# Kernel tuning notes

Measured on AMD Instinct MI355X. Metric: run time of the kernel, lower is better.

## Reference

```python
import jax, jax.numpy as jnp
import numpy as np

E, T, H, I = 16, 512, 1024, 4096


def setup_inputs() -> dict:
    key = jax.random.key(0)
    k_x, k_w1, k_b1, k_w2, k_b2 = jax.random.split(key, 5)
    scale = 0.02
    return {
        "route_results": jax.random.normal(k_x, (E, T, H), dtype=jnp.float32),
        "W1": jax.random.normal(k_w1, (E, H, I), dtype=jnp.float32) * scale,
        "b1": jax.random.normal(k_b1, (E, I), dtype=jnp.float32) * scale,
        "W2": jax.random.normal(k_w2, (E, I, H), dtype=jnp.float32) * scale,
        "b2": jax.random.normal(k_b2, (E, H), dtype=jnp.float32) * scale,
    }


def reference(route_results, W1, b1, W2, b2):
    # Per-expert 2-layer linear MLP (no activation in source), expressed as
    # a single grouped (batched) GEMM over the expert axis e.
    h = jnp.einsum("eth,ehi->eti", route_results, W1) + b1[:, None, :]
    y = jnp.einsum("eti,eih->eth", h, W2) + b2[:, None, :]
    # torch.cat(expert_results, dim=0): stack expert outputs along token dim.
    e, t, hid = y.shape
    return y.reshape(e * t, hid)
```

## Files before the change

kernel.cpp:

```cpp
#include <hip/hip_runtime.h>
#include <stdint.h>


#define E_ 16
#define T_ 512
#define H_ 1024
#define I_ 4096

typedef _Float16 f16x8 __attribute__((ext_vector_type(8)));
typedef __fp16   h2    __attribute__((ext_vector_type(2)));
typedef float    f32x4 __attribute__((ext_vector_type(4)));

#define LDK 40

__device__ __forceinline__ void lds_barrier() {
    __builtin_amdgcn_sched_barrier(0);
    asm volatile("s_waitcnt lgkmcnt(0)" ::: "memory");
    __builtin_amdgcn_sched_barrier(0);
    __builtin_amdgcn_s_barrier();
    __builtin_amdgcn_sched_barrier(0);
}

template <bool A_IS_F16, bool OUT_IS_F16>
__global__ __launch_bounds__(256, 2) void moe_gemm(const void* __restrict__ Aall,
                                                   const float* __restrict__ Ball,
                                                   const float* __restrict__ biasAll,
                                                   void* __restrict__ Call,
                                                   int M, int N, int K) {
    __shared__ _Float16 sA[2][128 * LDK];
    __shared__ _Float16 sB[2][128 * LDK];

    const int e   = blockIdx.z;
    const int m0  = blockIdx.y * 128;
    const int n0  = blockIdx.x * 128;
    const int tid = threadIdx.x;
    const int lane = tid & 63;
    const int wave = tid >> 6;
    const int wm = (wave >> 1) * 64;
    const int wn = (wave & 1) * 64;
    const int lrow = lane & 15;
    const int lk8  = (lane >> 4) * 8;

    const float* B_e    = Ball + (size_t)e * K * N;
    const float* bias_e = biasAll + (size_t)e * N;
    const float*     A_f32 = (const float*)Aall + (size_t)e * M * K;
    const _Float16*  A_f16 = (const _Float16*)Aall + (size_t)e * M * K;

    const int bn  = ((tid >> 6) & 1) * 64 + (tid & 63);
    const int bkh = (tid >> 7) * 16;
    const int ar = (tid >> 6) * 32 + ((tid & 63) >> 2);
    const int ak = (tid & 3) * 8;
    const int r  = tid >> 2;
    const int c8 = (tid & 3) * 8;

    float bv[16];
    f32x4 a32[4];
    f16x8 a16[2];

    auto load_tile = [&](int k0) {
        const float* bsrc = B_e + (size_t)(k0 + bkh) * N + n0 + bn;
#pragma unroll
        for (int kk = 0; kk < 16; ++kk)
            bv[kk] = bsrc[(size_t)kk * N];
        if (A_IS_F16) {
            a16[0] = *(const f16x8*)(A_f16 + (size_t)(m0 + r) * K + k0 + c8);
            a16[1] = *(const f16x8*)(A_f16 + (size_t)(m0 + r + 64) * K + k0 + c8);
        } else {
            const float* a0 = A_f32 + (size_t)(m0 + ar) * K + k0 + ak;
            a32[0] = *(const f32x4*)a0;
            a32[1] = *(const f32x4*)(a0 + 4);
            const float* a1 = A_f32 + (size_t)(m0 + ar + 16) * K + k0 + ak;
            a32[2] = *(const f32x4*)a1;
            a32[3] = *(const f32x4*)(a1 + 4);
        }
    };

    auto store_tile = [&](_Float16* dA, _Float16* dB) {
        f16x8 w0, w1;
#pragma unroll
        for (int j = 0; j < 4; ++j) {
            ((h2*)&w0)[j] = __builtin_amdgcn_cvt_pkrtz(bv[2 * j],     bv[2 * j + 1]);
            ((h2*)&w1)[j] = __builtin_amdgcn_cvt_pkrtz(bv[8 + 2 * j], bv[8 + 2 * j + 1]);
        }
        *(f16x8*)&dB[bn * LDK + bkh]     = w0;
        *(f16x8*)&dB[bn * LDK + bkh + 8] = w1;
        if (A_IS_F16) {
            *(f16x8*)&dA[r * LDK + c8]        = a16[0];
            *(f16x8*)&dA[(r + 64) * LDK + c8] = a16[1];
        } else {
#pragma unroll
            for (int p = 0; p < 2; ++p) {
                f16x8 w;
                ((h2*)&w)[0] = __builtin_amdgcn_cvt_pkrtz(a32[2 * p].x, a32[2 * p].y);
                ((h2*)&w)[1] = __builtin_amdgcn_cvt_pkrtz(a32[2 * p].z, a32[2 * p].w);
                ((h2*)&w)[2] = __builtin_amdgcn_cvt_pkrtz(a32[2 * p + 1].x, a32[2 * p + 1].y);
                ((h2*)&w)[3] = __builtin_amdgcn_cvt_pkrtz(a32[2 * p + 1].z, a32[2 * p + 1].w);
                *(f16x8*)&dA[(ar + p * 16) * LDK + ak] = w;
            }
        }
    };

    f32x4 acc[4][4];
    const f32x4 zero = {0.f, 0.f, 0.f, 0.f};
#pragma unroll
    for (int i = 0; i < 4; ++i)
#pragma unroll
        for (int j = 0; j < 4; ++j) acc[i][j] = zero;

    const int nt = K / 32;

    load_tile(0);
    store_tile(sA[0], sB[0]);
    load_tile(32);
    lds_barrier();

    for (int t = 0; t < nt; ++t) {
        const int cur = t & 1;
        const _Float16* rA = sA[cur];
        const _Float16* rB = sB[cur];

        f16x8 af[4], bf[4];
#pragma unroll
        for (int mi = 0; mi < 4; ++mi)
            af[mi] = *(const f16x8*)&rA[(wm + mi * 16 + lrow) * LDK + lk8];
#pragma unroll
        for (int ni = 0; ni < 4; ++ni)
            bf[ni] = *(const f16x8*)&rB[(wn + ni * 16 + lrow) * LDK + lk8];

#pragma unroll
        for (int mi = 0; mi < 2; ++mi)
#pragma unroll
            for (int ni = 0; ni < 4; ++ni)
                acc[mi][ni] = __builtin_amdgcn_mfma_f32_16x16x32_f16(af[mi], bf[ni], acc[mi][ni], 0, 0, 0);

        if (t + 1 < nt) {
            store_tile(sA[cur ^ 1], sB[cur ^ 1]);
            if (t + 2 < nt)
                load_tile((t + 2) * 32);
        }

#pragma unroll
        for (int mi = 2; mi < 4; ++mi)
#pragma unroll
            for (int ni = 0; ni < 4; ++ni)
                acc[mi][ni] = __builtin_amdgcn_mfma_f32_16x16x32_f16(af[mi], bf[ni], acc[mi][ni], 0, 0, 0);

        lds_barrier();
    }

    const int row_base = (lane >> 4) * 4;
#pragma unroll
    for (int ni = 0; ni < 4; ++ni) {
        const int n = n0 + wn + ni * 16 + lrow;
        const float bv2 = bias_e[n];
#pragma unroll
        for (int mi = 0; mi < 4; ++mi) {
            const int mbase = m0 + wm + mi * 16 + row_base;
#pragma unroll
            for (int rr = 0; rr < 4; ++rr) {
                const float val = acc[mi][ni][rr] + bv2;
                const size_t idx = (size_t)e * M * N + (size_t)(mbase + rr) * N + n;
                if (OUT_IS_F16)
                    ((_Float16*)Call)[idx] = (_Float16)val;
                else
                    ((float*)Call)[idx] = val;
            }
        }
    }
}

extern "C" void kernel_launch(void* const* d_in, const int* in_sizes, int n_in,
                              void* d_out, int out_size, void* d_ws, size_t ws_size,
                              hipStream_t stream) {
    (void)in_sizes; (void)n_in; (void)out_size; (void)ws_size;
    const float* x  = (const float*)d_in[0];
    const float* W1 = (const float*)d_in[1];
    const float* b1 = (const float*)d_in[2];
    const float* W2 = (const float*)d_in[3];
    const float* b2 = (const float*)d_in[4];
    float* out = (float*)d_out;
    _Float16* hbuf = (_Float16*)d_ws;

    dim3 blk(256, 1, 1);
    dim3 g1(I_ / 128, T_ / 128, E_);
    moe_gemm<false, true><<<g1, blk, 0, stream>>>((const void*)x, W1, b1, (void*)hbuf, T_, I_, H_);
    dim3 g2(H_ / 128, T_ / 128, E_);
    moe_gemm<true, false><<<g2, blk, 0, stream>>>((const void*)hbuf, W2, b2, (void*)out, T_, H_, I_);
}
```

Measured before the change: 695.8 us.

## Single-buffer LDS, raise occupancy, and use 64-row tiles for second GEMM

Replaces the double-buffered LDS pipeline with a single buffer and two barriers per k-step, so the LDS store of the next tile no longer overlaps the MFMA work. Launch bounds go from 2 to 4 blocks per CU, and the second GEMM uses BM=64 tiles, doubling its grid from 512 to 1024 blocks. The aim is better occupancy and wave parallelism on the second GEMM, at the cost of an extra barrier per iteration, lost intra-block overlap, and lower B-tile reuse per block.

```diff
diff --git a/kernel.cpp b/kernel.cpp
--- a/kernel.cpp
+++ b/kernel.cpp
@@ -21,22 +21,25 @@
     __builtin_amdgcn_sched_barrier(0);
 }
 
-template <bool A_IS_F16, bool OUT_IS_F16>
-__global__ __launch_bounds__(256, 2) void moe_gemm(const void* __restrict__ Aall,
+template <int BM, bool A_IS_F16, bool OUT_IS_F16>
+__global__ __launch_bounds__(256, 4) void moe_gemm(const void* __restrict__ Aall,
                                                    const float* __restrict__ Ball,
                                                    const float* __restrict__ biasAll,
                                                    void* __restrict__ Call,
                                                    int M, int N, int K) {
-    __shared__ _Float16 sA[2][128 * LDK];
-    __shared__ _Float16 sB[2][128 * LDK];
+    constexpr int MFRAG = BM / 32;
+    constexpr int AP    = BM / 64;
+
+    __shared__ _Float16 sA[BM * LDK];
+    __shared__ _Float16 sB[128 * LDK];
 
     const int e   = blockIdx.z;
-    const int m0  = blockIdx.y * 128;
+    const int m0  = blockIdx.y * BM;
     const int n0  = blockIdx.x * 128;
     const int tid = threadIdx.x;
     const int lane = tid & 63;
     const int wave = tid >> 6;
-    const int wm = (wave >> 1) * 64;
+    const int wm = (wave >> 1) * (BM / 2);
     const int wn = (wave & 1) * 64;
     const int lrow = lane & 15;
     const int lk8  = (lane >> 4) * 8;
@@ -46,16 +49,16 @@
     const float*     A_f32 = (const float*)Aall + (size_t)e * M * K;
     const _Float16*  A_f16 = (const _Float16*)Aall + (size_t)e * M * K;
 
-    const int bn  = ((tid >> 6) & 1) * 64 + (tid & 63);
+    const int bn  = tid & 127;
     const int bkh = (tid >> 7) * 16;
+    const int r  = tid >> 2;
+    const int c8 = (tid & 3) * 8;
     const int ar = (tid >> 6) * 32 + ((tid & 63) >> 2);
     const int ak = (tid & 3) * 8;
-    const int r  = tid >> 2;
-    const int c8 = (tid & 3) * 8;
 
     float bv[16];
-    f32x4 a32[4];
-    f16x8 a16[2];
+    f32x4 a32[2 * AP];
+    f16x8 a16[AP];
 
     auto load_tile = [&](int k0) {
         const float* bsrc = B_e + (size_t)(k0 + bkh) * N + n0 + bn;
@@ -63,102 +66,96 @@
         for (int kk = 0; kk < 16; ++kk)
             bv[kk] = bsrc[(size_t)kk * N];
         if (A_IS_F16) {
-            a16[0] = *(const f16x8*)(A_f16 + (size_t)(m0 + r) * K + k0 + c8);
-            a16[1] = *(const f16x8*)(A_f16 + (size_t)(m0 + r + 64) * K + k0 + c8);
+#pragma unroll
+            for (int p = 0; p < AP; ++p)
+                a16[p] = *(const f16x8*)(A_f16 + (size_t)(m0 + r + p * 64) * K + k0 + c8);
         } else {
-            const float* a0 = A_f32 + (size_t)(m0 + ar) * K + k0 + ak;
-            a32[0] = *(const f32x4*)a0;
-            a32[1] = *(const f32x4*)(a0 + 4);
-            const float* a1 = A_f32 + (size_t)(m0 + ar + 16) * K + k0 + ak;
-            a32[2] = *(const f32x4*)a1;
-            a32[3] = *(const f32x4*)(a1 + 4);
+#pragma unroll
+            for (int p = 0; p < AP; ++p) {
+                const int row = (BM == 128) ? (ar + p * 16) : (tid >> 2);
+                const float* a0 = A_f32 + (size_t)(m0 + row) * K + k0 + ak;
+                a32[2 * p]     = *(const f32x4*)a0;
+                a32[2 * p + 1] = *(const f32x4*)(a0 + 4);
+            }
         }
     };
 
-    auto store_tile = [&](_Float16* dA, _Float16* dB) {
+    auto store_tile = [&]() {
         f16x8 w0, w1;
 #pragma unroll
         for (int j = 0; j < 4; ++j) {
             ((h2*)&w0)[j] = __builtin_amdgcn_cvt_pkrtz(bv[2 * j],     bv[2 * j + 1]);
             ((h2*)&w1)[j] = __builtin_amdgcn_cvt_pkrtz(bv[8 + 2 * j], bv[8 + 2 * j + 1]);
         }
-        *(f16x8*)&dB[bn * LDK + bkh]     = w0;
-        *(f16x8*)&dB[bn * LDK + bkh + 8] = w1;
+        *(f16x8*)&sB[bn * LDK + bkh]     = w0;
+        *(f16x8*)&sB[bn * LDK + bkh + 8] = w1;
         if (A_IS_F16) {
-            *(f16x8*)&dA[r * LDK + c8]        = a16[0];
-            *(f16x8*)&dA[(r + 64) * LDK + c8] = a16[1];
+#pragma unroll
+            for (int p = 0; p < AP; ++p)
+                *(f16x8*)&sA[(r + p * 64) * LDK + c8] = a16[p];
         } else {
 #pragma unroll
-            for (int p = 0; p < 2; ++p) {
+            for (int p = 0; p < AP; ++p) {
+                const int row = (BM == 128) ? (ar + p * 16) : (tid >> 2);
                 f16x8 w;
                 ((h2*)&w)[0] = __builtin_amdgcn_cvt_pkrtz(a32[2 * p].x, a32[2 * p].y);
                 ((h2*)&w)[1] = __builtin_amdgcn_cvt_pkrtz(a32[2 * p].z, a32[2 * p].w);
                 ((h2*)&w)[2] = __builtin_amdgcn_cvt_pkrtz(a32[2 * p + 1].x, a32[2 * p + 1].y);
                 ((h2*)&w)[3] = __builtin_amdgcn_cvt_pkrtz(a32[2 * p + 1].z, a32[2 * p + 1].w);
-                *(f16x8*)&dA[(ar + p * 16) * LDK + ak] = w;
+                *(f16x8*)&sA[row * LDK + ak] = w;
             }
         }
     };
 
-    f32x4 acc[4][4];
+    f32x4 acc[MFRAG][4];
     const f32x4 zero = {0.f, 0.f, 0.f, 0.f};
 #pragma unroll
-    for (int i = 0; i < 4; ++i)
+    for (int i = 0; i < MFRAG; ++i)
 #pragma unroll
         for (int j = 0; j < 4; ++j) acc[i][j] = zero;
 
     const int nt = K / 32;
 
     load_tile(0);
-    store_tile(sA[0], sB[0]);
+    store_tile();
     load_tile(32);
     lds_barrier();
 
     for (int t = 0; t < nt; ++t) {
-        const int cur = t & 1;
-        const _Float16* rA = sA[cur];
-        const _Float16* rB = sB[cur];
-
-        f16x8 af[4], bf[4];
+        f16x8 af[MFRAG], bf[4];
 #pragma unroll
-        for (int mi = 0; mi < 4; ++mi)
-            af[mi] = *(const f16x8*)&rA[(wm + mi * 16 + lrow) * LDK + lk8];
+        for (int mi = 0; mi < MFRAG; ++mi)
+            af[mi] = *(const f16x8*)&sA[(wm + mi * 16 + lrow) * LDK + lk8];
 #pragma unroll
         for (int ni = 0; ni < 4; ++ni)
-            bf[ni] = *(const f16x8*)&rB[(wn + ni * 16 + lrow) * LDK + lk8];
-
+            bf[ni] = *(const f16x8*)&sB[(wn + ni * 16 + lrow) * LDK + lk8];
 #pragma unroll
-        for (int mi = 0; mi < 2; ++mi)
-#pragma unroll
-            for (int ni = 0; ni < 4; ++ni)
-                acc[mi][ni] = __builtin_amdgcn_mfma_f32_16x16x32_f16(af[mi], bf[ni], acc[mi][ni], 0, 0, 0);
-
-        if (t + 1 < nt) {
-            store_tile(sA[cur ^ 1], sB[cur ^ 1]);
-            if (t + 2 < nt)
-                load_tile((t + 2) * 32);
-        }
-
-#pragma unroll
-        for (int mi = 2; mi < 4; ++mi)
+        for (int mi = 0; mi < MFRAG; ++mi)
 #pragma unroll
             for (int ni = 0; ni < 4; ++ni)
                 acc[mi][ni] = __builtin_amdgcn_mfma_f32_16x16x32_f16(af[mi], bf[ni], acc[mi][ni], 0, 0, 0);
 
         lds_barrier();
+
+        if (t + 1 < nt) {
+            store_tile();
+            if (t + 2 < nt)
+                load_tile((t + 2) * 32);
+            lds_barrier();
+        }
     }
 
     const int row_base = (lane >> 4) * 4;
 #pragma unroll
     for (int ni = 0; ni < 4; ++ni) {
         const int n = n0 + wn + ni * 16 + lrow;
-        const float bv2 = bias_e[n];
+        const float bvx = bias_e[n];
 #pragma unroll
-        for (int mi = 0; mi < 4; ++mi) {
+        for (int mi = 0; mi < MFRAG; ++mi) {
             const int mbase = m0 + wm + mi * 16 + row_base;
 #pragma unroll
             for (int rr = 0; rr < 4; ++rr) {
-                const float val = acc[mi][ni][rr] + bv2;
+                const float val = acc[mi][ni][rr] + bvx;
                 const size_t idx = (size_t)e * M * N + (size_t)(mbase + rr) * N + n;
                 if (OUT_IS_F16)
                     ((_Float16*)Call)[idx] = (_Float16)val;
@@ -183,7 +180,7 @@
 
     dim3 blk(256, 1, 1);
     dim3 g1(I_ / 128, T_ / 128, E_);
-    moe_gemm<false, true><<<g1, blk, 0, stream>>>((const void*)x, W1, b1, (void*)hbuf, T_, I_, H_);
-    dim3 g2(H_ / 128, T_ / 128, E_);
-    moe_gemm<true, false><<<g2, blk, 0, stream>>>((const void*)hbuf, W2, b2, (void*)out, T_, H_, I_);
+    moe_gemm<128, false, true><<<g1, blk, 0, stream>>>((const void*)x, W1, b1, (void*)hbuf, T_, I_, H_);
+    dim3 g2(H_ / 128, T_ / 64, E_);
+    moe_gemm<64, true, false><<<g2, blk, 0, stream>>>((const void*)hbuf, W2, b2, (void*)out, T_, H_, I_);
 }
```

New measurement: 763.0 us. +9.7%, slower.
